# Kernel tuning notes

Hardware: AMD Instinct MI355X
Metric: run time of the kernel (lower is better)

Reference implementation:

```python
import jax, jax.numpy as jnp
import numpy as np

H, B, C, T, F = 4, 2, 64, 2048, 64   # n_head, batch, in_chan, time, n_freqs
HID = 4                               # hid_chan (per-head Q/K channels)
VD = C // H                           # per-head V channels
EPS = 1e-5


def prelu(x, a):
    return jnp.where(x >= 0, x, a * x)


def ln_cf(x, g, b):
    # LayerNormalization4D: normalize over (channel, freq) axes of (..., C, T, F)
    mu = x.mean(axis=(-3, -1), keepdims=True)
    var = ((x - mu) ** 2).mean(axis=(-3, -1), keepdims=True)
    return (x - mu) / jnp.sqrt(var + EPS) * g + b


def setup_inputs() -> dict:
    key = jax.random.key(0)
    ks = jax.random.split(key, 8)

    def w(k, shape):
        return jax.random.normal(k, shape, jnp.float32) * 0.05

    return {
        "x": jax.random.normal(ks[0], (B, C, T, F), jnp.float32),
        # per-head 1x1-conv Q/K/V projections (stacked over head axis)
        "Wq": w(ks[1], (H, HID, C)), "bq": jnp.zeros((H, HID), jnp.float32),
        "aq": jnp.full((H,), 0.25, jnp.float32),
        "gq": jnp.ones((H, HID, F), jnp.float32), "betq": jnp.zeros((H, HID, F), jnp.float32),
        "Wk": w(ks[2], (H, HID, C)), "bk": jnp.zeros((H, HID), jnp.float32),
        "ak": jnp.full((H,), 0.25, jnp.float32),
        "gk": jnp.ones((H, HID, F), jnp.float32), "betk": jnp.zeros((H, HID, F), jnp.float32),
        "Wv": w(ks[3], (H, VD, C)), "bv": jnp.zeros((H, VD), jnp.float32),
        "av": jnp.full((H,), 0.25, jnp.float32),
        "gv": jnp.ones((H, VD, F), jnp.float32), "betv": jnp.zeros((H, VD, F), jnp.float32),
        # output 1x1-conv projection
        "Wp": w(ks[4], (C, C)), "bp": jnp.zeros((C,), jnp.float32),
        "ap": jnp.full((), 0.25, jnp.float32),
        "gp": jnp.ones((C, F), jnp.float32), "betp": jnp.zeros((C, F), jnp.float32),
    }


def reference(x, Wq, bq, aq, gq, betq, Wk, bk, ak, gk, betk,
              Wv, bv, av, gv, betv, Wp, bp, ap, gp, betp):
    def qkv(W, b, a, g, be):
        # batched per-head 1x1 conv: (H,O,C) x (B,C,T,F) -> (H,B,O,T,F)
        y = jnp.einsum('hoc,bctf->hbotf', W, x) + b[:, None, :, None, None]
        y = prelu(y, a[:, None, None, None, None])
        return ln_cf(y, g[:, None, :, None, :], be[:, None, :, None, :])

    Q = qkv(Wq, bq, aq, gq, betq).reshape(H * B, HID, T, F)
    K = qkv(Wk, bk, ak, gk, betk).reshape(H * B, HID, T, F)
    V = qkv(Wv, bv, av, gv, betv).reshape(H * B, VD, T, F)

    # (HB, C', T, F) -> (HB, T, C'*F)
    Q = Q.transpose(0, 2, 1, 3).reshape(H * B, T, HID * F)
    K = K.transpose(0, 2, 1, 3).reshape(H * B, T, HID * F)
    V = V.transpose(0, 2, 1, 3).reshape(H * B, T, VD * F)

    scale = 1.0 / jnp.sqrt(jnp.asarray(HID * F, jnp.float32))
    attn = jax.nn.softmax(jnp.einsum('bqd,bkd->bqk', Q, K) * scale, axis=-1)  # (HB,T,T)
    O = jnp.einsum('bqk,bkd->bqd', attn, V)                                    # (HB,T,VD*F)

    # (HB,T,VD,F) -> (B, H*VD, T, F) matching torch head-concat order
    O = O.reshape(H * B, T, VD, F).transpose(0, 2, 1, 3)
    O = O.reshape(H, B, VD, T, F).transpose(1, 0, 2, 3, 4).reshape(B, H * VD, T, F)

    y = jnp.einsum('oc,bctf->botf', Wp, O) + bp[None, :, None, None]
    y = prelu(y, ap)
    y = ln_cf(y, gp[:, None, :], betp[:, None, :])
    return y + x
```

## Files before the change

### kernel.cpp

```cpp
#include <hip/hip_runtime.h>

#define EPS_ 1e-5f

typedef float f32x4 __attribute__((ext_vector_type(4)));
typedef short s16x8 __attribute__((ext_vector_type(8)));

static __device__ __forceinline__ short f2bf(float f) {
    unsigned u = __float_as_uint(f);
    unsigned r = (u + 0x7FFFu + ((u >> 16) & 1u)) >> 16;
    return (short)r;
}
static __device__ __forceinline__ float bf2f(short s) {
    return __uint_as_float(((unsigned)(unsigned short)s) << 16);
}

static __device__ __forceinline__ void gload16(const short* g, short* l) {
    __builtin_amdgcn_global_load_lds(
        (const __attribute__((address_space(1))) unsigned int*)g,
        (__attribute__((address_space(3))) unsigned int*)l, 16, 0, 0);
}

__global__ __launch_bounds__(256) void prep_kernel(
    const float* __restrict__ Wq, const float* __restrict__ Wk,
    const float* __restrict__ Wv, const float* __restrict__ Wp,
    short* __restrict__ Wbf, short* __restrict__ Wpbf)
{
    int i = blockIdx.x * 256 + threadIdx.x;
    if (i < 6144) {
        float v = (i < 1024) ? Wq[i] : (i < 2048 ? Wk[i - 1024] : Wv[i - 2048]);
        Wbf[i] = f2bf(v);
    } else if (i < 6144 + 4096) {
        Wpbf[i - 6144] = f2bf(Wp[i - 6144]);
    }
}

__global__ __launch_bounds__(256) void qkv_kernel(
    const float* __restrict__ x, const short* __restrict__ Wbf,
    const float* __restrict__ bq, const float* __restrict__ aq,
    const float* __restrict__ gq, const float* __restrict__ betq,
    const float* __restrict__ bk, const float* __restrict__ ak,
    const float* __restrict__ gk, const float* __restrict__ betk,
    const float* __restrict__ bv, const float* __restrict__ av,
    const float* __restrict__ gv, const float* __restrict__ betv,
    short* __restrict__ Qo, short* __restrict__ Ko, short* __restrict__ Vo)
{
    const int t = blockIdx.x;
    const int b = blockIdx.y;
    const int tid = threadIdx.x;
    const int wid = tid >> 6, lane = tid & 63;
    const int g = lane >> 4, c16 = lane & 15;
    const int f_ = tid & 63, cg = tid >> 6;

    __shared__ __align__(16) short wlds[96 * 64];
    __shared__ __align__(16) short xs[64 * 64];
    __shared__ float zs[96 * 64];
    __shared__ float stats[12][2];
    __shared__ float bias_l[96], alpha_l[96];

#pragma unroll
    for (int j = 0; j < 3; ++j) {
        int i8 = tid + 256 * j;
        int row = i8 >> 3, cb = i8 & 7;
        s16x8 v = *(const s16x8*)(Wbf + i8 * 8);
        *(s16x8*)&wlds[row * 64 + ((cb ^ (row & 7)) * 8)] = v;
    }
    if (tid < 96) {
        int row = tid; float bias, al;
        if (row < 16)      { bias = bq[row];      al = aq[row >> 2]; }
        else if (row < 32) { bias = bk[row - 16]; al = ak[(row - 16) >> 2]; }
        else               { bias = bv[row - 32]; al = av[(row - 32) >> 4]; }
        bias_l[row] = bias; alpha_l[row] = al;
    }
#pragma unroll
    for (int it = 0; it < 2; ++it) {
        int cb = cg + 4 * it, c0 = cb * 8;
        s16x8 v;
#pragma unroll
        for (int i = 0; i < 8; ++i)
            v[i] = f2bf(x[(((size_t)b * 64 + c0 + i) * 2048 + t) * 64 + f_]);
        *(s16x8*)&xs[f_ * 64 + ((cb ^ (f_ & 7)) * 8)] = v;
    }
    __syncthreads();

    const int f0 = wid * 16;
    s16x8 bfr[2];
#pragma unroll
    for (int kk = 0; kk < 2; ++kk)
        bfr[kk] = *(const s16x8*)&xs[(f0 + c16) * 64 + (((kk * 4 + g) ^ (c16 & 7)) * 8)];

    f32x4 acc[6];
#pragma unroll
    for (int rt = 0; rt < 6; ++rt) {
#pragma unroll
        for (int r = 0; r < 4; ++r) acc[rt][r] = 0.f;
#pragma unroll
        for (int kk = 0; kk < 2; ++kk) {
            s16x8 a = *(const s16x8*)&wlds[(rt * 16 + c16) * 64 + (((kk * 4 + g) ^ (c16 & 7)) * 8)];
            acc[rt] = __builtin_amdgcn_mfma_f32_16x16x32_bf16(a, bfr[kk], acc[rt], 0, 0, 0);
        }
    }

#pragma unroll
    for (int rt = 0; rt < 6; ++rt)
#pragma unroll
        for (int r = 0; r < 4; ++r) {
            int row = rt * 16 + g * 4 + r;
            float z = acc[rt][r] + bias_l[row];
            z = z >= 0.f ? z : alpha_l[row] * z;
            zs[row * 64 + f0 + c16] = z;
        }
    __syncthreads();

#pragma unroll
    for (int gi = 0; gi < 3; ++gi) {
        int grp = wid * 3 + gi;
        int base_row, n;
        if (grp < 4)      { base_row = grp * 4;             n = 256; }
        else if (grp < 8) { base_row = 16 + (grp - 4) * 4;  n = 256; }
        else              { base_row = 32 + (grp - 8) * 16; n = 1024; }
        int cnt = n >> 6;
        float s = 0.f, ss = 0.f;
        for (int i = 0; i < cnt; ++i) {
            float v = zs[(base_row + i) * 64 + lane];
            s += v; ss += v * v;
        }
#pragma unroll
        for (int msk = 32; msk >= 1; msk >>= 1) {
            s  += __shfl_xor(s, msk);
            ss += __shfl_xor(ss, msk);
        }
        if (lane == 0) {
            float mean = s / n;
            float var = ss / n - mean * mean;
            stats[grp][0] = mean;
            stats[grp][1] = rsqrtf(var + EPS_);
        }
    }
    __syncthreads();

#pragma unroll
    for (int j = 0; j < 24; ++j) {
        int row = cg + 4 * j;
        float zv = zs[row * 64 + f_];
        if (row < 16) {
            int grp = row >> 2;
            float val = (zv - stats[grp][0]) * stats[grp][1];
            val = val * gq[row * 64 + f_] + betq[row * 64 + f_];
            int h = row >> 2, o = row & 3;
            Qo[(((size_t)(h * 2 + b)) * 2048 + t) * 256 + o * 64 + f_] = f2bf(val);
        } else if (row < 32) {
            int rr = row - 16, grp = 4 + (rr >> 2);
            float val = (zv - stats[grp][0]) * stats[grp][1];
            val = val * gk[rr * 64 + f_] + betk[rr * 64 + f_];
            int h = rr >> 2, o = rr & 3;
            Ko[(((size_t)(h * 2 + b)) * 2048 + t) * 256 + o * 64 + f_] = f2bf(val);
        } else {
            int rr = row - 32, grp = 8 + (rr >> 4);
            float val = (zv - stats[grp][0]) * stats[grp][1];
            val = val * gv[rr * 64 + f_] + betv[rr * 64 + f_];
            int h = rr >> 4, ov = rr & 15;
            Vo[(((size_t)(h * 2 + b)) * 2048 + t) * 1024 + ov * 64 + f_] = f2bf(val);
        }
    }
}

__global__ __launch_bounds__(256) void vtrans_kernel(
    const short* __restrict__ Vrm, short* __restrict__ Vt)
{
    const int t0 = blockIdx.x * 64;
    const int d0 = blockIdx.y * 64;
    const int hb = blockIdx.z;
    const int tid = threadIdx.x;
    __shared__ __align__(16) short tile[64 * 72];

#pragma unroll
    for (int k = 0; k < 2; ++k) {
        int q = tid + 256 * k;
        int row = q >> 3, slot = q & 7;
        s16x8 v = *(const s16x8*)(Vrm + ((size_t)hb * 2048 + t0 + row) * 1024 + d0 + slot * 8);
        *(s16x8*)&tile[row * 72 + slot * 8] = v;
    }
    __syncthreads();
#pragma unroll
    for (int k = 0; k < 2; ++k) {
        int q = tid + 256 * k;
        int drow = q >> 3, tslot = q & 7;
        s16x8 v;
#pragma unroll
        for (int i = 0; i < 8; ++i) {
            int c = tslot * 8 + i;
            int cl = c & 31;
            int src = (c & 32) + ((cl >> 2) & 1) * 16 + ((cl >> 4) & 1) * 8
                    + ((cl >> 3) & 1) * 4 + (cl & 3);
            v[i] = tile[src * 72 + drow];
        }
        *(s16x8*)(Vt + ((size_t)hb * 1024 + d0 + drow) * 2048 + t0 + tslot * 8) = v;
    }
}

__global__ __launch_bounds__(512, 2) void attn_kernel(
    const short* __restrict__ Qg, const short* __restrict__ Kg,
    const short* __restrict__ Vt, short* __restrict__ Ob)
{
    const int hb = blockIdx.x;
    const int qt = blockIdx.y;
    const int dh = blockIdx.z;
    const int t0 = qt * 128;
    const int tid = threadIdx.x;
    const int lane = tid & 63;
    const int wid = tid >> 6;
    const int g = lane >> 4, c16 = lane & 15;

    __shared__ __align__(16) short k_lds[2][32 * 256];
    __shared__ __align__(16) short v_lds[2][512 * 32];
    __shared__ __align__(16) short p_lds[2][8][512];
    __shared__ float l_sh[128];

    const size_t kgbase = (size_t)hb * 2048 * 256;
    const size_t vgbase = ((size_t)hb * 1024 + dh * 512) * 2048;
    const int dsl = wid * 64;

    const size_t qrow = (size_t)hb * 2048 + t0 + wid * 16 + c16;
    s16x8 qf[8];
#pragma unroll
    for (int kf = 0; kf < 8; ++kf)
        qf[kf] = *(const s16x8*)(Qg + qrow * 256 + kf * 32 + g * 8);

    f32x4 oacc[32];
#pragma unroll
    for (int i = 0; i < 32; ++i)
#pragma unroll
        for (int r = 0; r < 4; ++r) oacc[i][r] = 0.f;

    float l_r = 0.f;

#define STAGE_K(buf, kt) do {                                                  \
    _Pragma("unroll")                                                          \
    for (int j_ = 0; j_ < 2; ++j_) {                                           \
        int c_ = tid + 512 * j_;                                               \
        int row_ = c_ >> 5, sp_ = c_ & 31;                                     \
        int sl_ = sp_ ^ (row_ & 7);                                            \
        gload16(Kg + kgbase + (size_t)((kt) * 32 + row_) * 256 + sl_ * 8,      \
                &k_lds[buf][c_ * 8]);                                          \
    }                                                                          \
} while (0)

#define STAGE_V(buf, kt) do {                                                  \
    _Pragma("unroll")                                                          \
    for (int j_ = 0; j_ < 4; ++j_) {                                           \
        int c_ = tid + 512 * j_;                                               \
        int row_ = c_ >> 2, sp_ = c_ & 3;                                      \
        int sl_ = sp_ ^ ((row_ >> 1) & 3);                                     \
        gload16(Vt + vgbase + (size_t)row_ * 2048 + (kt) * 32 + sl_ * 8,       \
                &v_lds[buf][c_ * 8]);                                          \
    }                                                                          \
} while (0)

#define QKT_PHASE(nt) do {                                                     \
    f32x4 sf0, sf1;                                                            \
    _Pragma("unroll")                                                          \
    for (int r = 0; r < 4; ++r) { sf0[r] = 0.f; sf1[r] = 0.f; }                \
    __builtin_amdgcn_s_setprio(1);                                             \
    _Pragma("unroll")                                                          \
    for (int kf = 0; kf < 8; ++kf) {                                           \
        int sl_ = ((kf * 4 + g) ^ (c16 & 7)) * 8;                              \
        s16x8 ka0 = *(const s16x8*)&k_lds[(nt) & 1][c16 * 256 + sl_];          \
        sf0 = __builtin_amdgcn_mfma_f32_16x16x32_bf16(ka0, qf[kf], sf0, 0, 0, 0); \
        s16x8 ka1 = *(const s16x8*)&k_lds[(nt) & 1][(16 + c16) * 256 + sl_];   \
        sf1 = __builtin_amdgcn_mfma_f32_16x16x32_bf16(ka1, qf[kf], sf1, 0, 0, 0); \
    }                                                                          \
    __builtin_amdgcn_s_setprio(0);                                             \
    float rs = 0.f;                                                            \
    _Pragma("unroll")                                                          \
    for (int r = 0; r < 4; ++r) {                                              \
        float p0 = __expf(sf0[r] * 0.0625f);                                   \
        float p1 = __expf(sf1[r] * 0.0625f);                                   \
        sf0[r] = p0; sf1[r] = p1;                                              \
        rs += p0 + p1;                                                         \
    }                                                                          \
    rs += __shfl_xor(rs, 16);                                                  \
    rs += __shfl_xor(rs, 32);                                                  \
    l_r += rs;                                                                 \
    s16x8 pa;                                                                  \
    _Pragma("unroll")                                                          \
    for (int e = 0; e < 8; ++e)                                                \
        pa[e] = f2bf((e & 4) ? sf1[e & 3] : sf0[e & 3]);                       \
    *(s16x8*)&p_lds[(nt) & 1][wid][lane * 8] = pa;                             \
} while (0)

    STAGE_K(0, 0);
    __syncthreads();
    STAGE_K(1, 1);
    STAGE_V(0, 0);
    QKT_PHASE(0);
    __syncthreads();

    for (int t = 0; t < 64; ++t) {
        const int buf = t & 1;

        if (t < 62) STAGE_K(buf, t + 2);
        if (t < 63) STAGE_V(buf ^ 1, t + 1);
        if (t < 63) QKT_PHASE(t + 1);

        s16x8 vb[4];
#pragma unroll
        for (int dt = 0; dt < 4; ++dt) {
            int rowv = dsl + dt * 16 + c16;
            vb[dt] = *(const s16x8*)&v_lds[buf][rowv * 32 + ((g ^ ((c16 >> 1) & 3)) * 8)];
        }
        __builtin_amdgcn_s_setprio(1);
#pragma unroll
        for (int qs = 0; qs < 8; ++qs) {
            s16x8 pa = *(const s16x8*)&p_lds[buf][qs][lane * 8];
#pragma unroll
            for (int dt = 0; dt < 4; ++dt)
                oacc[qs * 4 + dt] = __builtin_amdgcn_mfma_f32_16x16x32_bf16(
                    pa, vb[dt], oacc[qs * 4 + dt], 0, 0, 0);
        }
        __builtin_amdgcn_s_setprio(0);

        if (t < 63) __syncthreads();
    }

#undef STAGE_K
#undef STAGE_V
#undef QKT_PHASE

    __syncthreads();
    if (lane < 16) l_sh[wid * 16 + lane] = l_r;
    __syncthreads();

    const int h = hb >> 1, b = hb & 1;
#pragma unroll
    for (int qs = 0; qs < 8; ++qs) {
        float li[4];
#pragma unroll
        for (int r = 0; r < 4; ++r)
            li[r] = 1.f / l_sh[qs * 16 + g * 4 + r];
#pragma unroll
        for (int dt = 0; dt < 4; ++dt) {
            int vcol = dh * 512 + dsl + dt * 16 + c16;
            int cout = h * 16 + (vcol >> 6), ff = vcol & 63;
#pragma unroll
            for (int r = 0; r < 4; ++r) {
                int trow = t0 + qs * 16 + g * 4 + r;
                Ob[(((size_t)b * 64 + cout) * 2048 + trow) * 64 + ff] =
                    f2bf(oacc[qs * 4 + dt][r] * li[r]);
            }
        }
    }
}

__global__ __launch_bounds__(256) void oproj_kernel(
    const short* __restrict__ Ob, const float* __restrict__ x,
    const short* __restrict__ Wpbf,
    const float* __restrict__ bp, const float* __restrict__ ap,
    const float* __restrict__ gp, const float* __restrict__ betp,
    float* __restrict__ out)
{
    const int t = blockIdx.x;
    const int b = blockIdx.y;
    const int tid = threadIdx.x;
    const int wid = tid >> 6, lane = tid & 63;
    const int g = lane >> 4, c16 = lane & 15;
    const int f_ = tid & 63, cg = tid >> 6;

    __shared__ __align__(16) short wp[64 * 64];
    __shared__ __align__(16) short os[64 * 64];
    __shared__ float zs[64 * 64];
    __shared__ float red[4][2];

#pragma unroll
    for (int j = 0; j < 2; ++j) {
        int i8 = tid + 256 * j;
        int row = i8 >> 3, cb = i8 & 7;
        s16x8 v = *(const s16x8*)(Wpbf + i8 * 8);
        *(s16x8*)&wp[row * 64 + ((cb ^ (row & 7)) * 8)] = v;
    }
#pragma unroll
    for (int it = 0; it < 2; ++it) {
        int cb = cg + 4 * it, c0 = cb * 8;
        s16x8 v;
#pragma unroll
        for (int i = 0; i < 8; ++i)
            v[i] = Ob[(((size_t)b * 64 + c0 + i) * 2048 + t) * 64 + f_];
        *(s16x8*)&os[f_ * 64 + ((cb ^ (f_ & 7)) * 8)] = v;
    }
    __syncthreads();

    const int f0 = wid * 16;
    s16x8 bfr[2];
#pragma unroll
    for (int kk = 0; kk < 2; ++kk)
        bfr[kk] = *(const s16x8*)&os[(f0 + c16) * 64 + (((kk * 4 + g) ^ (c16 & 7)) * 8)];

    const float ap0 = ap[0];
    f32x4 acc[4];
#pragma unroll
    for (int rt = 0; rt < 4; ++rt) {
#pragma unroll
        for (int r = 0; r < 4; ++r) acc[rt][r] = 0.f;
#pragma unroll
        for (int kk = 0; kk < 2; ++kk) {
            s16x8 a = *(const s16x8*)&wp[(rt * 16 + c16) * 64 + (((kk * 4 + g) ^ (c16 & 7)) * 8)];
            acc[rt] = __builtin_amdgcn_mfma_f32_16x16x32_bf16(a, bfr[kk], acc[rt], 0, 0, 0);
        }
    }

#pragma unroll
    for (int rt = 0; rt < 4; ++rt)
#pragma unroll
        for (int r = 0; r < 4; ++r) {
            int row = rt * 16 + g * 4 + r;
            float z = acc[rt][r] + bp[row];
            z = z >= 0.f ? z : ap0 * z;
            zs[row * 64 + f0 + c16] = z;
        }
    __syncthreads();

    float s = 0.f, ss = 0.f;
#pragma unroll
    for (int j = 0; j < 16; ++j) {
        float v = zs[(cg + 4 * j) * 64 + f_];
        s += v; ss += v * v;
    }
#pragma unroll
    for (int msk = 32; msk >= 1; msk >>= 1) {
        s  += __shfl_xor(s, msk);
        ss += __shfl_xor(ss, msk);
    }
    if (lane == 0) { red[wid][0] = s; red[wid][1] = ss; }
    __syncthreads();
    float ts  = red[0][0] + red[1][0] + red[2][0] + red[3][0];
    float tss = red[0][1] + red[1][1] + red[2][1] + red[3][1];
    float mean = ts * (1.f / 4096.f);
    float rstd = rsqrtf(tss * (1.f / 4096.f) - mean * mean + EPS_);

#pragma unroll
    for (int j = 0; j < 16; ++j) {
        int row = cg + 4 * j;
        size_t idx = (((size_t)b * 64 + row) * 2048 + t) * 64 + f_;
        out[idx] = (zs[row * 64 + f_] - mean) * rstd * gp[row * 64 + f_]
                 + betp[row * 64 + f_] + x[idx];
    }
}

extern "C" void kernel_launch(void* const* d_in, const int* in_sizes, int n_in,
                              void* d_out, int out_size, void* d_ws, size_t ws_size,
                              hipStream_t stream)
{
    const float* x    = (const float*)d_in[0];
    const float* Wq   = (const float*)d_in[1];
    const float* bq   = (const float*)d_in[2];
    const float* aq   = (const float*)d_in[3];
    const float* gq   = (const float*)d_in[4];
    const float* betq = (const float*)d_in[5];
    const float* Wk   = (const float*)d_in[6];
    const float* bk   = (const float*)d_in[7];
    const float* ak   = (const float*)d_in[8];
    const float* gk   = (const float*)d_in[9];
    const float* betk = (const float*)d_in[10];
    const float* Wv   = (const float*)d_in[11];
    const float* bv   = (const float*)d_in[12];
    const float* av   = (const float*)d_in[13];
    const float* gv   = (const float*)d_in[14];
    const float* betv = (const float*)d_in[15];
    const float* Wp   = (const float*)d_in[16];
    const float* bp   = (const float*)d_in[17];
    const float* ap   = (const float*)d_in[18];
    const float* gp   = (const float*)d_in[19];
    const float* betp = (const float*)d_in[20];

    short* Qb   = (short*)d_ws;
    short* Kb   = Qb   + (size_t)8 * 2048 * 256;
    short* Vrm  = Kb   + (size_t)8 * 2048 * 256;
    short* Vt   = Vrm  + (size_t)8 * 2048 * 1024;
    short* Obuf = Vt   + (size_t)8 * 2048 * 1024;
    short* Wbf  = Obuf + (size_t)8 * 2048 * 1024;
    short* Wpbf = Wbf  + 96 * 64;

    prep_kernel<<<40, 256, 0, stream>>>(Wq, Wk, Wv, Wp, Wbf, Wpbf);
    qkv_kernel<<<dim3(2048, 2), 256, 0, stream>>>(x, Wbf,
        bq, aq, gq, betq, bk, ak, gk, betk, bv, av, gv, betv, Qb, Kb, Vrm);
    vtrans_kernel<<<dim3(32, 16, 8), 256, 0, stream>>>(Vrm, Vt);
    attn_kernel<<<dim3(8, 16, 2), 512, 0, stream>>>(Qb, Kb, Vt, Obuf);
    oproj_kernel<<<dim3(2048, 2), 256, 0, stream>>>(Obuf, x, Wpbf,
        bp, ap, gp, betp, (float*)d_out);
}
```

Before: 240.0 us.

## Restructure attention tiling: full-D per block, V fragments loaded directly from global

The attention kernel now covers all 1024 V columns per block with 64 query rows, instead of splitting D across two blocks with 128 query rows. This removes the duplicated QK^T/softmax work across the D split. Key tiles grow to 64, and the waves split the key range in half and sum the row sums at the end. V is no longer staged through LDS; each wave reads its V fragments straight from global memory into registers, which frees LDS but makes PV depend on global latency and scattered loads.

```diff
diff --git a/kernel.cpp b/kernel.cpp
--- a/kernel.cpp
+++ b/kernel.cpp
@@ -204,23 +204,23 @@
 {
     const int hb = blockIdx.x;
     const int qt = blockIdx.y;
-    const int dh = blockIdx.z;
-    const int t0 = qt * 128;
+    const int t0 = qt * 64;
     const int tid = threadIdx.x;
     const int lane = tid & 63;
     const int wid = tid >> 6;
+    const int qs = wid >> 1;
+    const int kp = wid & 1;
     const int g = lane >> 4, c16 = lane & 15;
 
-    __shared__ __align__(16) short k_lds[2][32 * 256];
-    __shared__ __align__(16) short v_lds[2][512 * 32];
-    __shared__ __align__(16) short p_lds[2][8][512];
-    __shared__ float l_sh[128];
+    __shared__ __align__(16) short k_lds[2][64 * 256];
+    __shared__ __align__(16) short p_lds[2][4][2][512];
+    __shared__ float l_sh[2][64];
 
     const size_t kgbase = (size_t)hb * 2048 * 256;
-    const size_t vgbase = ((size_t)hb * 1024 + dh * 512) * 2048;
-    const int dsl = wid * 64;
-
-    const size_t qrow = (size_t)hb * 2048 + t0 + wid * 16 + c16;
+    const size_t vgbase = (size_t)hb * 1024 * 2048;
+    const int dsl = wid * 128;
+
+    const size_t qrow = (size_t)hb * 2048 + t0 + qs * 16 + c16;
     s16x8 qf[8];
 #pragma unroll
     for (int kf = 0; kf < 8; ++kf)
@@ -236,23 +236,12 @@
 
 #define STAGE_K(buf, kt) do {                                                  \
     _Pragma("unroll")                                                          \
-    for (int j_ = 0; j_ < 2; ++j_) {                                           \
+    for (int j_ = 0; j_ < 4; ++j_) {                                           \
         int c_ = tid + 512 * j_;                                               \
         int row_ = c_ >> 5, sp_ = c_ & 31;                                     \
         int sl_ = sp_ ^ (row_ & 7);                                            \
-        gload16(Kg + kgbase + (size_t)((kt) * 32 + row_) * 256 + sl_ * 8,      \
+        gload16(Kg + kgbase + (size_t)((kt) * 64 + row_) * 256 + sl_ * 8,      \
                 &k_lds[buf][c_ * 8]);                                          \
-    }                                                                          \
-} while (0)
-
-#define STAGE_V(buf, kt) do {                                                  \
-    _Pragma("unroll")                                                          \
-    for (int j_ = 0; j_ < 4; ++j_) {                                           \
-        int c_ = tid + 512 * j_;                                               \
-        int row_ = c_ >> 2, sp_ = c_ & 3;                                      \
-        int sl_ = sp_ ^ ((row_ >> 1) & 3);                                     \
-        gload16(Vt + vgbase + (size_t)row_ * 2048 + (kt) * 32 + sl_ * 8,       \
-                &v_lds[buf][c_ * 8]);                                          \
     }                                                                          \
 } while (0)
 
@@ -264,9 +253,9 @@
     _Pragma("unroll")                                                          \
     for (int kf = 0; kf < 8; ++kf) {                                           \
         int sl_ = ((kf * 4 + g) ^ (c16 & 7)) * 8;                              \
-        s16x8 ka0 = *(const s16x8*)&k_lds[(nt) & 1][c16 * 256 + sl_];          \
+        s16x8 ka0 = *(const s16x8*)&k_lds[(nt) & 1][(kp * 32 + c16) * 256 + sl_]; \
         sf0 = __builtin_amdgcn_mfma_f32_16x16x32_bf16(ka0, qf[kf], sf0, 0, 0, 0); \
-        s16x8 ka1 = *(const s16x8*)&k_lds[(nt) & 1][(16 + c16) * 256 + sl_];   \
+        s16x8 ka1 = *(const s16x8*)&k_lds[(nt) & 1][(kp * 32 + 16 + c16) * 256 + sl_]; \
         sf1 = __builtin_amdgcn_mfma_f32_16x16x32_bf16(ka1, qf[kf], sf1, 0, 0, 0); \
     }                                                                          \
     __builtin_amdgcn_s_setprio(0);                                             \
@@ -285,67 +274,73 @@
     _Pragma("unroll")                                                          \
     for (int e = 0; e < 8; ++e)                                                \
         pa[e] = f2bf((e & 4) ? sf1[e & 3] : sf0[e & 3]);                       \
-    *(s16x8*)&p_lds[(nt) & 1][wid][lane * 8] = pa;                             \
+    *(s16x8*)&p_lds[(nt) & 1][qs][kp][lane * 8] = pa;                          \
 } while (0)
 
     STAGE_K(0, 0);
     __syncthreads();
     STAGE_K(1, 1);
-    STAGE_V(0, 0);
     QKT_PHASE(0);
     __syncthreads();
 
-    for (int t = 0; t < 64; ++t) {
+    for (int t = 0; t < 32; ++t) {
         const int buf = t & 1;
-
-        if (t < 62) STAGE_K(buf, t + 2);
-        if (t < 63) STAGE_V(buf ^ 1, t + 1);
-        if (t < 63) QKT_PHASE(t + 1);
-
-        s16x8 vb[4];
-#pragma unroll
-        for (int dt = 0; dt < 4; ++dt) {
-            int rowv = dsl + dt * 16 + c16;
-            vb[dt] = *(const s16x8*)&v_lds[buf][rowv * 32 + ((g ^ ((c16 >> 1) & 3)) * 8)];
-        }
-        __builtin_amdgcn_s_setprio(1);
-#pragma unroll
-        for (int qs = 0; qs < 8; ++qs) {
-            s16x8 pa = *(const s16x8*)&p_lds[buf][qs][lane * 8];
-#pragma unroll
-            for (int dt = 0; dt < 4; ++dt)
-                oacc[qs * 4 + dt] = __builtin_amdgcn_mfma_f32_16x16x32_bf16(
-                    pa, vb[dt], oacc[qs * 4 + dt], 0, 0, 0);
-        }
-        __builtin_amdgcn_s_setprio(0);
-
-        if (t < 63) __syncthreads();
+        const int kt0 = t * 64;
+
+        s16x8 vf[8][2];
+#pragma unroll
+        for (int dt = 0; dt < 8; ++dt)
+#pragma unroll
+            for (int k2 = 0; k2 < 2; ++k2)
+                vf[dt][k2] = *(const s16x8*)(Vt + vgbase
+                    + (size_t)(dsl + dt * 16 + c16) * 2048 + kt0 + k2 * 32 + g * 8);
+
+        if (t < 30) STAGE_K(buf, t + 2);
+        if (t < 31) QKT_PHASE(t + 1);
+
+#pragma unroll
+        for (int q2 = 0; q2 < 4; ++q2) {
+            s16x8 pa0 = *(const s16x8*)&p_lds[buf][q2][0][lane * 8];
+            s16x8 pa1 = *(const s16x8*)&p_lds[buf][q2][1][lane * 8];
+            __builtin_amdgcn_s_setprio(1);
+#pragma unroll
+            for (int dt = 0; dt < 8; ++dt) {
+                oacc[q2 * 8 + dt] = __builtin_amdgcn_mfma_f32_16x16x32_bf16(
+                    pa0, vf[dt][0], oacc[q2 * 8 + dt], 0, 0, 0);
+                oacc[q2 * 8 + dt] = __builtin_amdgcn_mfma_f32_16x16x32_bf16(
+                    pa1, vf[dt][1], oacc[q2 * 8 + dt], 0, 0, 0);
+            }
+            __builtin_amdgcn_s_setprio(0);
+        }
+
+        if (t < 31) __syncthreads();
     }
 
 #undef STAGE_K
-#undef STAGE_V
 #undef QKT_PHASE
 
     __syncthreads();
-    if (lane < 16) l_sh[wid * 16 + lane] = l_r;
+    if (lane < 16) l_sh[kp][qs * 16 + lane] = l_r;
     __syncthreads();
 
     const int h = hb >> 1, b = hb & 1;
 #pragma unroll
-    for (int qs = 0; qs < 8; ++qs) {
+    for (int q2 = 0; q2 < 4; ++q2) {
         float li[4];
 #pragma unroll
-        for (int r = 0; r < 4; ++r)
-            li[r] = 1.f / l_sh[qs * 16 + g * 4 + r];
-#pragma unroll
-        for (int dt = 0; dt < 4; ++dt) {
-            int vcol = dh * 512 + dsl + dt * 16 + c16;
+        for (int r = 0; r < 4; ++r) {
+            int row = q2 * 16 + g * 4 + r;
+            li[r] = 1.f / (l_sh[0][row] + l_sh[1][row]);
+        }
+#pragma unroll
+        for (int dt = 0; dt < 8; ++dt) {
+            int vcol = dsl + dt * 16 + c16;
             int cout = h * 16 + (vcol >> 6), ff = vcol & 63;
 #pragma unroll
             for (int r = 0; r < 4; ++r) {
-                int trow = t0 + qs * 16 + g * 4 + r;
+                int trow = t0 + q2 * 16 + g * 4 + r;
                 Ob[(((size_t)b * 64 + cout) * 2048 + trow) * 64 + ff] =
-                    f2bf(oacc[qs * 4 + dt][r] * li[r]);
+                    f2bf(oacc[q2 * 8 + dt][r] * li[r]);
             }
         }
     }
@@ -483,7 +478,7 @@
     qkv_kernel<<<dim3(2048, 2), 256, 0, stream>>>(x, Wbf,
         bq, aq, gq, betq, bk, ak, gk, betk, bv, av, gv, betv, Qb, Kb, Vrm);
     vtrans_kernel<<<dim3(32, 16, 8), 256, 0, stream>>>(Vrm, Vt);
-    attn_kernel<<<dim3(8, 16, 2), 512, 0, stream>>>(Qb, Kb, Vt, Obuf);
+    attn_kernel<<<dim3(8, 32), 512, 0, stream>>>(Qb, Kb, Vt, Obuf);
     oproj_kernel<<<dim3(2048, 2), 256, 0, stream>>>(Obuf, x, Wpbf,
         bp, ap, gp, betp, (float*)d_out);
 }
```

Result: slower. 332.4 us (+38.5%).
